# Optimization experiments

Hardware: AMD Instinct MI355X
Metric: run time of the kernel (lower is better)

The kernel has to match this reference:

```python
import jax, jax.numpy as jnp
import numpy as np

EPS = 1e-05  # eigenvalue clamp, from module __init__ default


def setup_inputs() -> dict:
    key = jax.random.key(0)
    B, C = 8192, 64
    A = jax.random.normal(key, (B, C, C), dtype=jnp.float32)
    # Build well-conditioned SPD matrices: S = A A^T / C + 1e-3 I
    S = jnp.einsum('bij,bkj->bik', A, A) / C + 1e-3 * jnp.eye(C, dtype=jnp.float32)
    return {"S": S}


def reference(S) -> jnp.ndarray:
    """Log-Euclidean map: S = Q diag(w) Q^T -> Q diag(log(max(w, eps))) Q^T.

    Faithful to SPDLogMap.forward: compute in float32, clamp eigenvalues at eps,
    cast result back to the input dtype.
    """
    orig_dtype = S.dtype
    Sf = S.astype(jnp.float32)
    w, v = jnp.linalg.eigh(Sf)                      # w: (B, C), v: (B, C, C)
    log_w = jnp.log(jnp.maximum(w, EPS))            # clamp then log
    # Q diag(log_w) Q^T without materializing diag_embed
    result = jnp.einsum('bic,bc,bjc->bij', v, log_w, v)
    return result.astype(orig_dtype)
```

## Files before the change

### kernel.cpp

```cpp
#include <hip/hip_runtime.h>
#include <math.h>

#define NSWEEP_MAX 16
#define T2_TOL 2e-9f
#define EPS2 1e-10f


__device__ __forceinline__ float bperm_f(int idx, float x) {
    return __int_as_float(__builtin_amdgcn_ds_bpermute(idx, __float_as_int(x)));
}
__device__ __forceinline__ float rdlane_f(float x, int l) {
    return __int_as_float(__builtin_amdgcn_readlane(__float_as_int(x), l));
}

__global__ __launch_bounds__(64, 2) void spdlog_onesided(
    const float* __restrict__ S, float* __restrict__ Out, int nmat) {
    __shared__ float X[64][64];
    const int lane = threadIdx.x;
    const int b = blockIdx.x;
    if (b >= nmat) return;
    const float* Sb = S + (size_t)b * 4096;
    float* Ob = Out + (size_t)b * 4096;

    float g[64];
    #pragma unroll 64
    for (int s = 0; s < 64; ++s) g[s] = Sb[s * 64 + lane];

    float dpp = 0.0f;

    #pragma unroll 1
    for (int sweep = 0; sweep < NSWEEP_MAX; ++sweep) {
        dpp = 0.0f;
        #pragma unroll 64
        for (int s = 0; s < 64; ++s) dpp = fmaf(g[s], g[s], dpp);

        float maxt2 = 0.0f;
        #pragma unroll 1
        for (int m = 1; m < 64; ++m) {
            const int xl = lane ^ m;
            const int idx = xl << 2;
            const bool isLow = lane < xl;
            float pr[64];
            float dpq = 0.0f;
            #pragma unroll 64
            for (int s = 0; s < 64; ++s) {
                pr[s] = bperm_f(idx, g[s]);
                dpq = fmaf(g[s], pr[s], dpq);
            }
            const float pd = bperm_f(idx, dpp);
            const float d_lo = isLow ? dpp : pd;
            const float d_hi = isLow ? pd : dpp;
            const float t2 = dpq * dpq * __builtin_amdgcn_rcpf(dpp * pd);
            maxt2 = fmaxf(maxt2, t2);
            const float tau = (d_hi - d_lo) * __builtin_amdgcn_rcpf(2.0f * dpq);
            const float sq = __builtin_amdgcn_sqrtf(fmaf(tau, tau, 1.0f));
            float tt = __builtin_amdgcn_rcpf(fabsf(tau) + sq);
            tt = copysignf(tt, tau);
            float cc = __builtin_amdgcn_rsqf(fmaf(tt, tt, 1.0f));
            float ss = tt * cc;
            const bool tiny = fabsf(dpq) < 1e-30f;
            cc = tiny ? 1.0f : cc;
            ss = tiny ? 0.0f : ss;
            tt = tiny ? 0.0f : tt;
            const float es = isLow ? -ss : ss;
            const float t_own = isLow ? tt : -tt;
            dpp = fmaf(-t_own, dpq, dpp);
            #pragma unroll 64
            for (int s = 0; s < 64; ++s) g[s] = fmaf(cc, g[s], es * pr[s]);
        }
        maxt2 = fmaxf(maxt2, __shfl_xor(maxt2, 1));
        maxt2 = fmaxf(maxt2, __shfl_xor(maxt2, 2));
        maxt2 = fmaxf(maxt2, __shfl_xor(maxt2, 4));
        maxt2 = fmaxf(maxt2, __shfl_xor(maxt2, 8));
        maxt2 = fmaxf(maxt2, __shfl_xor(maxt2, 16));
        maxt2 = fmaxf(maxt2, __shfl_xor(maxt2, 32));
        if (maxt2 < T2_TOL) break;
    }

    float dfin = 0.0f;
    #pragma unroll 64
    for (int s = 0; s < 64; ++s) dfin = fmaf(g[s], g[s], dfin);
    const float w = 0.5f * logf(fmaxf(dfin, EPS2));
    const float rs = __builtin_amdgcn_rsqf(fmaxf(dfin, 1e-20f));

    #pragma unroll 64
    for (int s = 0; s < 64; ++s) X[s][lane] = g[s] * rs;
    __syncthreads();
    float uw[64];
    {
        const float4* rowp = (const float4*)&X[lane][0];
        #pragma unroll 16
        for (int gq = 0; gq < 16; ++gq) {
            const float4 q = rowp[gq];
            uw[4 * gq + 0] = q.x;
            uw[4 * gq + 1] = q.y;
            uw[4 * gq + 2] = q.z;
            uw[4 * gq + 3] = q.w;
        }
    }
    #pragma unroll 64
    for (int c = 0; c < 64; ++c) uw[c] *= rdlane_f(w, c);
    #pragma unroll 2
    for (int i = 0; i < 64; ++i) {
        const float4* Urow = (const float4*)&X[i][0];
        float acc = 0.0f;
        #pragma unroll 16
        for (int gq = 0; gq < 16; ++gq) {
            const float4 q = Urow[gq];
            acc = fmaf(q.x, uw[4 * gq + 0], acc);
            acc = fmaf(q.y, uw[4 * gq + 1], acc);
            acc = fmaf(q.z, uw[4 * gq + 2], acc);
            acc = fmaf(q.w, uw[4 * gq + 3], acc);
        }
        Ob[i * 64 + lane] = acc;
    }
}

extern "C" void kernel_launch(void* const* d_in, const int* in_sizes, int n_in,
                              void* d_out, int out_size, void* d_ws, size_t ws_size,
                              hipStream_t stream) {
    const float* S = (const float*)d_in[0];
    float* Out = (float*)d_out;
    const int nmat = in_sizes[0] / 4096;
    spdlog_onesided<<<nmat, 64, 0, stream>>>(S, Out, nmat);
}
```

Before: 4.352 ms.

## Replace bpermute Jacobi pairing with DPP/permlane Gray-code partner walk and skip converged rotations

Walks the partner lane along a Gray-code sequence so each step's partner is reached from the previous partner's data by a cheap DPP move or permlane swap. The partner copy is carried and rotated alongside the lane's own column, which replaces 64 ds_bpermute LDS round trips per pairing step. Rotations are skipped wave-wide when every pair is already below tolerance. The convergence tolerance is loosened 100x, which cuts sweeps but can reduce eigenvector accuracy. Occupancy is lowered to one wave per SIMD to fit the extra partner registers.

```diff
diff --git a/kernel.cpp b/kernel.cpp
--- a/kernel.cpp
+++ b/kernel.cpp
@@ -2,18 +2,145 @@
 #include <math.h>
 
 #define NSWEEP_MAX 16
-#define T2_TOL 2e-9f
+#define T2_TOL 2e-7f
 #define EPS2 1e-10f
 
 
-__device__ __forceinline__ float bperm_f(int idx, float x) {
-    return __int_as_float(__builtin_amdgcn_ds_bpermute(idx, __float_as_int(x)));
-}
+#define RMASK " row_mask:0xf bank_mask:0xf"
+#define X1S "quad_perm:[1,0,3,2]" RMASK
+#define X2S "quad_perm:[2,3,0,1]" RMASK
+#define X7S "row_half_mirror" RMASK
+#define X8S "row_ror:8" RMASK
+
+__constant__ int c_delta[63] = {
+    0, 2, 1, 7, 1, 2, 1, 8, 1, 2, 1, 7, 1, 2, 1,
+    16, 1, 2, 1, 7, 1, 2, 1, 8, 1, 2, 1, 7, 1, 2, 1,
+    32, 1, 2, 1, 7, 1, 2, 1, 8, 1, 2, 1, 7, 1, 2, 1,
+    16, 1, 2, 1, 7, 1, 2, 1, 8, 1, 2, 1, 7, 1, 2, 1};
+
 __device__ __forceinline__ float rdlane_f(float x, int l) {
     return __int_as_float(__builtin_amdgcn_readlane(__float_as_int(x), l));
 }
 
-__global__ __launch_bounds__(64, 2) void spdlog_onesided(
+#define COEFF_BLOCK                                                        \
+    const int xl = lane ^ mcur;                                            \
+    const bool isLow = lane < xl;                                          \
+    const float d_lo = isLow ? dO : pd;                                    \
+    const float d_hi = isLow ? pd : dO;                                    \
+    const float tau = (d_hi - d_lo) * __builtin_amdgcn_rcpf(2.0f * dpq);   \
+    const float sqv = __builtin_amdgcn_sqrtf(fmaf(tau, tau, 1.0f));        \
+    float tt = __builtin_amdgcn_rcpf(fabsf(tau) + sqv);                    \
+    tt = copysignf(tt, tau);                                               \
+    float cc = __builtin_amdgcn_rsqf(fmaf(tt, tt, 1.0f));                  \
+    float ss = tt * cc;                                                    \
+    const bool tiny = fabsf(dpq) < 1e-30f;                                 \
+    cc = tiny ? 1.0f : cc;                                                 \
+    ss = tiny ? 0.0f : ss;                                                 \
+    tt = tiny ? 0.0f : tt;                                                 \
+    const float es = isLow ? -ss : ss;                                     \
+    const float nes = -es;                                                 \
+    const float t_own = isLow ? tt : -tt;                                  \
+    const float pdn = fmaf(t_own, dpq, pd);                                \
+    dO = fmaf(-t_own, dpq, dO);                                            \
+    pd = pdn;
+
+#define JR(CS)                                                             \
+    {                                                                      \
+        asm volatile("s_nop 1");                                           \
+        asm volatile("v_mov_b32_dpp %0, %0 " CS : "+v"(pd));               \
+        float a0 = 0.f, a1 = 0.f, a2 = 0.f, a3 = 0.f;                      \
+        _Pragma("unroll") for (int s = 0; s < 64; s += 4) {                \
+            asm volatile("v_fmac_f32_dpp %0, %1, %2 " CS                   \
+                         : "+v"(a0) : "v"(pr[s + 0]), "v"(g[s + 0]));      \
+            asm volatile("v_fmac_f32_dpp %0, %1, %2 " CS                   \
+                         : "+v"(a1) : "v"(pr[s + 1]), "v"(g[s + 1]));      \
+            asm volatile("v_fmac_f32_dpp %0, %1, %2 " CS                   \
+                         : "+v"(a2) : "v"(pr[s + 2]), "v"(g[s + 2]));      \
+            asm volatile("v_fmac_f32_dpp %0, %1, %2 " CS                   \
+                         : "+v"(a3) : "v"(pr[s + 3]), "v"(g[s + 3]));      \
+        }                                                                  \
+        const float dpq = (a0 + a1) + (a2 + a3);                           \
+        const float t2 = dpq * dpq * __builtin_amdgcn_rcpf(dO * pd);       \
+        maxt2 = fmaxf(maxt2, t2);                                          \
+        if (__all(t2 < T2_TOL)) {                                          \
+            _Pragma("unroll") for (int s = 0; s < 64; ++s)                 \
+                asm volatile("v_mov_b32_dpp %0, %0 " CS : "+v"(pr[s]));    \
+        } else {                                                           \
+            COEFF_BLOCK                                                    \
+            _Pragma("unroll") for (int s = 0; s < 64; s += 4) {            \
+                float m0, m1v, m2v, m3, t0, t1, t2v, t3;                   \
+                asm volatile("v_mul_f32_dpp %0, %1, %2 " CS                \
+                             : "=v"(m0) : "v"(pr[s + 0]), "v"(es));        \
+                asm volatile("v_mul_f32_dpp %0, %1, %2 " CS                \
+                             : "=v"(m1v) : "v"(pr[s + 1]), "v"(es));       \
+                asm volatile("v_mul_f32_dpp %0, %1, %2 " CS                \
+                             : "=v"(m2v) : "v"(pr[s + 2]), "v"(es));       \
+                asm volatile("v_mul_f32_dpp %0, %1, %2 " CS                \
+                             : "=v"(m3) : "v"(pr[s + 3]), "v"(es));        \
+                asm volatile("v_mul_f32 %0, %1, %2"                        \
+                             : "=v"(t0) : "v"(g[s + 0]), "v"(nes));        \
+                asm volatile("v_mul_f32 %0, %1, %2"                        \
+                             : "=v"(t1) : "v"(g[s + 1]), "v"(nes));        \
+                asm volatile("v_mul_f32 %0, %1, %2"                        \
+                             : "=v"(t2v) : "v"(g[s + 2]), "v"(nes));       \
+                asm volatile("v_mul_f32 %0, %1, %2"                        \
+                             : "=v"(t3) : "v"(g[s + 3]), "v"(nes));        \
+                asm volatile("v_fmac_f32_dpp %0, %1, %2 " CS               \
+                             : "+v"(t0) : "v"(pr[s + 0]), "v"(cc));        \
+                asm volatile("v_fmac_f32_dpp %0, %1, %2 " CS               \
+                             : "+v"(t1) : "v"(pr[s + 1]), "v"(cc));        \
+                asm volatile("v_fmac_f32_dpp %0, %1, %2 " CS               \
+                             : "+v"(t2v) : "v"(pr[s + 2]), "v"(cc));       \
+                asm volatile("v_fmac_f32_dpp %0, %1, %2 " CS               \
+                             : "+v"(t3) : "v"(pr[s + 3]), "v"(cc));        \
+                g[s + 0] = fmaf(cc, g[s + 0], m0);                         \
+                g[s + 1] = fmaf(cc, g[s + 1], m1v);                        \
+                g[s + 2] = fmaf(cc, g[s + 2], m2v);                        \
+                g[s + 3] = fmaf(cc, g[s + 3], m3);                         \
+                pr[s + 0] = t0;                                            \
+                pr[s + 1] = t1;                                            \
+                pr[s + 2] = t2v;                                           \
+                pr[s + 3] = t3;                                            \
+            }                                                              \
+        }                                                                  \
+        __builtin_amdgcn_sched_barrier(0);                                 \
+    }
+
+#define JR_BODY_PLAIN                                                      \
+    {                                                                      \
+        float a0 = 0.f, a1 = 0.f, a2 = 0.f, a3 = 0.f;                      \
+        _Pragma("unroll") for (int s = 0; s < 64; s += 4) {                \
+            a0 = fmaf(g[s + 0], pr[s + 0], a0);                            \
+            a1 = fmaf(g[s + 1], pr[s + 1], a1);                            \
+            a2 = fmaf(g[s + 2], pr[s + 2], a2);                            \
+            a3 = fmaf(g[s + 3], pr[s + 3], a3);                            \
+        }                                                                  \
+        const float dpq = (a0 + a1) + (a2 + a3);                           \
+        const float t2 = dpq * dpq * __builtin_amdgcn_rcpf(dO * pd);       \
+        maxt2 = fmaxf(maxt2, t2);                                          \
+        if (!__all(t2 < T2_TOL)) {                                         \
+            COEFF_BLOCK                                                    \
+            _Pragma("unroll") for (int s = 0; s < 64; ++s) {               \
+                const float m1 = es * pr[s];                               \
+                const float t = nes * g[s];                                \
+                g[s] = fmaf(cc, g[s], m1);                                 \
+                pr[s] = fmaf(cc, pr[s], t);                                \
+            }                                                              \
+        }                                                                  \
+        __builtin_amdgcn_sched_barrier(0);                                 \
+    }
+
+#define JR_SWAP(NBITS)                                                     \
+    {                                                                      \
+        asm volatile("s_nop 1");                                           \
+        asm volatile("v_permlane" #NBITS "_swap_b32 %0, %0" : "+v"(pd));   \
+        _Pragma("unroll") for (int s = 0; s < 64; ++s)                     \
+            asm volatile("v_permlane" #NBITS "_swap_b32 %0, %0"            \
+                         : "+v"(pr[s]));                                   \
+        JR_BODY_PLAIN                                                      \
+    }
+
+__global__ __launch_bounds__(64, 1) void spdlog_onesided(
     const float* __restrict__ S, float* __restrict__ Out, int nmat) {
     __shared__ float X[64][64];
     const int lane = threadIdx.x;
@@ -26,47 +153,46 @@
     #pragma unroll 64
     for (int s = 0; s < 64; ++s) g[s] = Sb[s * 64 + lane];
 
-    float dpp = 0.0f;
+    float dO = 0.0f;
 
     #pragma unroll 1
     for (int sweep = 0; sweep < NSWEEP_MAX; ++sweep) {
-        dpp = 0.0f;
+        {
+            float d0 = 0.f, d1 = 0.f, d2 = 0.f, d3 = 0.f;
+            #pragma unroll 16
+            for (int s = 0; s < 64; s += 4) {
+                d0 = fmaf(g[s], g[s], d0);
+                d1 = fmaf(g[s + 1], g[s + 1], d1);
+                d2 = fmaf(g[s + 2], g[s + 2], d2);
+                d3 = fmaf(g[s + 3], g[s + 3], d3);
+            }
+            dO = (d0 + d1) + (d2 + d3);
+        }
+        __builtin_amdgcn_sched_barrier(0);
+        asm volatile("s_nop 1");
+        float pd;
+        asm volatile("v_mov_b32_dpp %0, %1 " X1S : "=v"(pd) : "v"(dO));
+        float pr[64];
         #pragma unroll 64
-        for (int s = 0; s < 64; ++s) dpp = fmaf(g[s], g[s], dpp);
-
+        for (int s = 0; s < 64; ++s)
+            asm volatile("v_mov_b32_dpp %0, %1 " X1S : "=v"(pr[s]) : "v"(g[s]));
+        __builtin_amdgcn_sched_barrier(0);
+
+        int mcur = 1;
         float maxt2 = 0.0f;
         #pragma unroll 1
-        for (int m = 1; m < 64; ++m) {
-            const int xl = lane ^ m;
-            const int idx = xl << 2;
-            const bool isLow = lane < xl;
-            float pr[64];
-            float dpq = 0.0f;
-            #pragma unroll 64
-            for (int s = 0; s < 64; ++s) {
-                pr[s] = bperm_f(idx, g[s]);
-                dpq = fmaf(g[s], pr[s], dpq);
+        for (int t = 0; t < 63; ++t) {
+            const int delta = c_delta[t];
+            mcur ^= delta;
+            switch (delta) {
+                case 0: JR_BODY_PLAIN break;
+                case 1: JR(X1S) break;
+                case 2: JR(X2S) break;
+                case 7: JR(X7S) break;
+                case 8: JR(X8S) break;
+                case 16: JR_SWAP(16) break;
+                default: JR_SWAP(32) break;
             }
-            const float pd = bperm_f(idx, dpp);
-            const float d_lo = isLow ? dpp : pd;
-            const float d_hi = isLow ? pd : dpp;
-            const float t2 = dpq * dpq * __builtin_amdgcn_rcpf(dpp * pd);
-            maxt2 = fmaxf(maxt2, t2);
-            const float tau = (d_hi - d_lo) * __builtin_amdgcn_rcpf(2.0f * dpq);
-            const float sq = __builtin_amdgcn_sqrtf(fmaf(tau, tau, 1.0f));
-            float tt = __builtin_amdgcn_rcpf(fabsf(tau) + sq);
-            tt = copysignf(tt, tau);
-            float cc = __builtin_amdgcn_rsqf(fmaf(tt, tt, 1.0f));
-            float ss = tt * cc;
-            const bool tiny = fabsf(dpq) < 1e-30f;
-            cc = tiny ? 1.0f : cc;
-            ss = tiny ? 0.0f : ss;
-            tt = tiny ? 0.0f : tt;
-            const float es = isLow ? -ss : ss;
-            const float t_own = isLow ? tt : -tt;
-            dpp = fmaf(-t_own, dpq, dpp);
-            #pragma unroll 64
-            for (int s = 0; s < 64; ++s) g[s] = fmaf(cc, g[s], es * pr[s]);
         }
         maxt2 = fmaxf(maxt2, __shfl_xor(maxt2, 1));
         maxt2 = fmaxf(maxt2, __shfl_xor(maxt2, 2));
```

Result: slower. 7.409 ms (+70.2%).
